# Kernel tuning notes

Hardware: AMD Instinct MI355X
Metric: run time of the kernel (lower is better)

Reference implementation:

```python
import math
import jax, jax.numpy as jnp
import numpy as np

B, T, C = 4, 2048, 1024
N_HEAD = 16
HEAD_DIM = C // N_HEAD

def setup_inputs() -> dict:
    key = jax.random.key(0)
    k0, k1, k2, k3, k4 = jax.random.split(key, 5)
    s = 1.0 / math.sqrt(C)
    return {
        "x": jax.random.normal(k0, (B, T, C), dtype=jnp.float32),
        "W_q": jax.random.normal(k1, (C, C), dtype=jnp.float32) * s,
        "W_k": jax.random.normal(k2, (C, C), dtype=jnp.float32) * s,
        "W_v": jax.random.normal(k3, (C, C), dtype=jnp.float32) * s,
        "W_o": jax.random.normal(k4, (C, C), dtype=jnp.float32) * s,
    }

def reference(x, W_q, W_k, W_v, W_o):
    b, t, c = x.shape
    h, hd = N_HEAD, HEAD_DIM
    # nn.Linear(y) = y @ W.T ; project and split heads -> [B, H, T, hd]
    q = (x @ W_q.T).reshape(b, t, h, hd).transpose(0, 2, 1, 3)
    k = (x @ W_k.T).reshape(b, t, h, hd).transpose(0, 2, 1, 3)
    v = (x @ W_v.T).reshape(b, t, h, hd).transpose(0, 2, 1, 3)
    # scores [B, H, T, T], causal mask, stable softmax
    attn = jnp.einsum('bhqd,bhkd->bhqk', q, k) / math.sqrt(hd)
    causal = jnp.tril(jnp.ones((t, t), dtype=bool))
    attn = jnp.where(causal[None, None], attn, -jnp.inf)
    attn = jax.nn.softmax(attn, axis=-1)
    out = jnp.einsum('bhqk,bhkd->bhqd', attn, v)
    out = out.transpose(0, 2, 1, 3).reshape(b, t, c)
    return out @ W_o.T
```

## Files before the change

kernel.cpp:

```cpp
#include <hip/hip_runtime.h>
#include <math.h>

#define Bsz 4
#define Tsz 2048
#define Csz 1024
#define NH  16
#define HD  64

typedef short bf16x8 __attribute__((ext_vector_type(8)));
typedef float f32x4  __attribute__((ext_vector_type(4)));
typedef unsigned short u16;
typedef unsigned int uint;

__device__ __forceinline__ u16 f2bf(float f) {
    union { float f; unsigned u; } v; v.f = f;
    unsigned r = v.u + 0x7fffu + ((v.u >> 16) & 1u);
    return (u16)(r >> 16);
}

__device__ __forceinline__ uint pkbf(float a, float b) {
    union { float f; uint u; } x, y; x.f = a; y.f = b;
    return ((x.u + 0x8000u) >> 16) | ((y.u + 0x8000u) & 0xFFFF0000u);
}

__device__ __forceinline__ void glds16(const u16* g, u16* l) {
    __builtin_amdgcn_global_load_lds(
        (const __attribute__((address_space(1))) void*)g,
        (__attribute__((address_space(3))) void*)l, 16, 0, 0);
}

__global__ void cast_all(const float* __restrict__ x,
                         const float* __restrict__ s0, const float* __restrict__ s1,
                         const float* __restrict__ s2, const float* __restrict__ s3,
                         u16* __restrict__ xb, u16* __restrict__ wdst) {
    const int NW = Csz * Csz;
    const size_t NX = (size_t)Bsz * Tsz * Csz;
    size_t i = ((size_t)blockIdx.x * blockDim.x + threadIdx.x) * 8;
    const float* src;
    u16* dst;
    if (i < NX) {
        src = x + i; dst = xb + i;
    } else {
        size_t j = i - NX;
        int m = (int)(j >> 20);
        size_t local = j & (NW - 1);
        src = ((m == 0) ? s0 : (m == 1) ? s1 : (m == 2) ? s2 : s3) + local;
        dst = wdst + j;
    }
    float4 a = *(const float4*)(src);
    float4 b = *(const float4*)(src + 4);
    bf16x8 o;
    o[0] = (short)f2bf(a.x); o[1] = (short)f2bf(a.y);
    o[2] = (short)f2bf(a.z); o[3] = (short)f2bf(a.w);
    o[4] = (short)f2bf(b.x); o[5] = (short)f2bf(b.y);
    o[6] = (short)f2bf(b.z); o[7] = (short)f2bf(b.w);
    *(bf16x8*)(dst) = o;
}


#define G2_SS 24576

#define G2_STAGEA(SLOT, KH, KT, PTR) {                                               \
    const int row_ = tid >> 2;                                                       \
    const int sc_ = (tid & 3) ^ ((row_ >> 1) & 3);                                   \
    glds16((PTR) + (size_t)row_ * 1024 + (KT) * 64 + (KH) * 32 + sc_ * 8,            \
           lds + (SLOT) * G2_SS + (KH) * 4096 + wave * 512); }

#define G2_STAGEB(SLOT, KH, KT, PTR) {                                               \
    _Pragma("unroll")                                                                \
    for (int rho = 0; rho < 2; rho++) {                                              \
        const int row_ = rho * 128 + (tid >> 2);                                     \
        const int sc_ = (tid & 3) ^ ((row_ >> 1) & 3);                               \
        glds16((PTR) + (size_t)row_ * 1024 + (KT) * 64 + (KH) * 32 + sc_ * 8,        \
               lds + (SLOT) * G2_SS + 8192 + (KH) * 8192 + rho * 4096 + wave * 512); } }

#define G2_PHASE(SLOT, KH, STAGE)                                                    \
    {                                                                                \
        __builtin_amdgcn_s_barrier();                                                \
        asm volatile("" ::: "memory");                                               \
        STAGE                                                                        \
        const u16* abase = lds + (SLOT) * G2_SS + (KH) * 4096;                       \
        const u16* bbase = lds + (SLOT) * G2_SS + 8192 + (KH) * 8192;                \
        bf16x8 afr[4], bfr[4];                                                       \
        _Pragma("unroll")                                                            \
        for (int i = 0; i < 4; i++) {                                                \
            const int ar = wrb + i * 16 + lr;                                        \
            afr[i] = *(const bf16x8*)(abase + ar * 32 +                              \
                                      ((lq ^ ((ar >> 1) & 3)) * 8));                 \
        }                                                                            \
        _Pragma("unroll")                                                            \
        for (int j = 0; j < 4; j++) {                                                \
            const int nr = wcb + j * 16 + lr;                                        \
            bfr[j] = *(const bf16x8*)(bbase + nr * 32 +                              \
                                      ((lq ^ ((nr >> 1) & 3)) * 8));                 \
        }                                                                            \
        asm volatile("" ::: "memory");                                               \
        __builtin_amdgcn_s_setprio(1);                                               \
        _Pragma("unroll")                                                            \
        for (int i = 0; i < 4; i++)                                                  \
            _Pragma("unroll")                                                        \
            for (int j = 0; j < 4; j++)                                              \
                acc[i][j] = __builtin_amdgcn_mfma_f32_16x16x32_bf16(                 \
                    afr[i], bfr[j], acc[i][j], 0, 0, 0);                             \
        __builtin_amdgcn_s_setprio(0);                                               \
    }

#define G2_VM(N) asm volatile("s_waitcnt vmcnt(" #N ")" ::: "memory")

#define G2_BODY(AP_, BP_)                                                            \
    __shared__ u16 lds[49152];                                                       \
    const int tid = threadIdx.x;                                                     \
    const int wave = tid >> 6, lane = tid & 63;                                      \
    const int lr = lane & 15, lq = lane >> 4;                                        \
    const int wrb = (wave >> 2) * 64, wcb = (wave & 3) * 64;                         \
    f32x4 acc[4][4] = {};                                                            \
    G2_STAGEA(0, 0, 0, AP_) G2_STAGEB(0, 0, 0, BP_)                                  \
    G2_STAGEA(0, 1, 0, AP_) G2_STAGEB(0, 1, 0, BP_)                                  \
    G2_STAGEA(1, 0, 1, AP_) G2_STAGEB(1, 0, 1, BP_)                                  \
    for (int t = 0; t < 16; t++) {                                                   \
        const int s = t & 1;                                                         \
        if (t == 15) { G2_VM(3); } else { G2_VM(6); }                                \
        G2_PHASE(s, 0, if (t < 15) { G2_STAGEA(s ^ 1, 1, t + 1, AP_)                 \
                                     G2_STAGEB(s ^ 1, 1, t + 1, BP_) })              \
        if (t == 15) { G2_VM(0); } else { G2_VM(6); }                                \
        G2_PHASE(s, 1, if (t < 14) { G2_STAGEA(s, 0, t + 2, AP_)                     \
                                     G2_STAGEB(s, 0, t + 2, BP_) })                  \
    }

__global__ __launch_bounds__(512, 2)
void gemm_qkv(const u16* __restrict__ A, const u16* __restrict__ Bm,
              u16* __restrict__ Qo, u16* __restrict__ Ko, u16* __restrict__ Vo,
              float qscale) {
    const int wg = blockIdx.x;
    const int chunk = wg & 7, pos = wg >> 3;
    const int m0 = ((chunk >> 1) * 16 + pos / 6) * 128;
    const int n0 = ((chunk & 1) * 6 + pos % 6) * 256;
    const u16* Ap = A  + (size_t)m0 * 1024;
    const u16* Bp = Bm + (size_t)n0 * 1024;

    G2_BODY(Ap, Bp)

    const int sel = n0 >> 10;
    if (sel == 2) {
        #pragma unroll
        for (int mi = 0; mi < 4; mi++) {
            #pragma unroll
            for (int ni = 0; ni < 4; ni++) {
                int m = m0 + wrb + mi * 16 + lq * 4;
                int b = m >> 11, tt = m & (Tsz - 1);
                int n = (n0 & 1023) + wcb + ni * 16 + lr;
                int h = n >> 6, d = n & (HD - 1);
                uint2 pk;
                pk.x = pkbf(acc[mi][ni][0], acc[mi][ni][1]);
                pk.y = pkbf(acc[mi][ni][2], acc[mi][ni][3]);
                *(uint2*)(&Vo[(((size_t)b * NH + h) * HD + d) * Tsz + tt]) = pk;
            }
        }
    } else {
        const float scale = (sel == 0) ? qscale : 1.0f;
        u16* dst = (sel == 0) ? Qo : Ko;
        #pragma unroll
        for (int mi = 0; mi < 4; mi++)
            #pragma unroll
            for (int ni = 0; ni < 4; ni++)
                #pragma unroll
                for (int r = 0; r < 4; r++) {
                    int m = m0 + wrb + mi * 16 + lq * 4 + r;
                    int n = (n0 & 1023) + wcb + ni * 16 + lr;
                    int b = m >> 11, tt = m & (Tsz - 1);
                    int h = n >> 6,  d = n & (HD - 1);
                    dst[(((size_t)b * NH + h) * Tsz + tt) * HD + d] = f2bf(acc[mi][ni][r] * scale);
                }
    }
}

__global__ __launch_bounds__(512, 2)
void gemm_out(const u16* __restrict__ A, const u16* __restrict__ Bm,
              float* __restrict__ out) {
    const int wg = blockIdx.x;
    const int chunk = wg & 7, pos = wg >> 3;
    const int m0 = (chunk * 8 + (pos >> 2)) * 128;
    const int n0 = (pos & 3) * 256;
    const u16* Ap = A  + (size_t)m0 * 1024;
    const u16* Bp = Bm + (size_t)n0 * 1024;

    G2_BODY(Ap, Bp)

    #pragma unroll
    for (int mi = 0; mi < 4; mi++)
        #pragma unroll
        for (int ni = 0; ni < 4; ni++)
            #pragma unroll
            for (int r = 0; r < 4; r++) {
                int m = m0 + wrb + mi * 16 + lq * 4 + r;
                int n = n0 + wcb + ni * 16 + lr;
                out[(size_t)m * Csz + n] = acc[mi][ni][r];
            }
}

#define LDT  72
#define LDTP 68

__global__ __launch_bounds__(256, 4)
void attn_kernel(const u16* __restrict__ Q, const u16* __restrict__ Kb,
                 const u16* __restrict__ Vt, u16* __restrict__ O) {
    __shared__ u16 sK[64 * LDT];
    __shared__ u16 sV[64 * LDT];
    __shared__ u16 sP[4][16 * LDTP];
    const int tid  = threadIdx.x;
    const int wave = tid >> 6, lane = tid & 63;
    const int lr = lane & 15, lq = lane >> 4;
    const int bh = blockIdx.x;
    const int qa = blockIdx.y;
    const int qc = 31 - qa;
    const int ta = qa * 64, tc = qc * 64;

    const u16* Qp = Q  + (size_t)bh * Tsz * HD;
    const u16* Kp = Kb + (size_t)bh * Tsz * HD;
    const u16* Vp = Vt + (size_t)bh * HD * Tsz;

    bf16x8 qfA0 = *(const bf16x8*)(Qp + (size_t)(ta + wave * 16 + lr) * HD + lq * 8);
    bf16x8 qfA1 = *(const bf16x8*)(Qp + (size_t)(ta + wave * 16 + lr) * HD + 32 + lq * 8);
    bf16x8 qfC0 = *(const bf16x8*)(Qp + (size_t)(tc + wave * 16 + lr) * HD + lq * 8);
    bf16x8 qfC1 = *(const bf16x8*)(Qp + (size_t)(tc + wave * 16 + lr) * HD + 32 + lq * 8);

    f32x4 accOA[4] = {}, accOC[4] = {};
    f32x4 accLA = {}, accLC = {};

    bf16x8 ones;
    #pragma unroll
    for (int i = 0; i < 8; i++) ones[i] = (short)0x3F80;

    const int strow = tid >> 3;
    const int stcol = (tid & 7) * 8;
    const u16* gK0 = Kp + (size_t)strow * HD + stcol;
    const u16* gK1 = gK0 + 32 * HD;
    const u16* gV0 = Vp + (size_t)strow * Tsz + stcol;
    const u16* gV1 = gV0 + 32 * Tsz;
    u16* lK0 = sK + strow * LDT + stcol;  u16* lK1 = lK0 + 32 * LDT;
    u16* lV0 = sV + strow * LDT + stcol;  u16* lV1 = lV0 + 32 * LDT;

    bf16x8 pK0 = *(const bf16x8*)(gK0);
    bf16x8 pK1 = *(const bf16x8*)(gK1);
    bf16x8 pV0 = *(const bf16x8*)(gV0);
    bf16x8 pV1 = *(const bf16x8*)(gV1);

#define PROCESS(T0, QF0, QF1, ACCO, ACCL, DIAG)                                       \
    {                                                                                 \
        f32x4 accS[4];                                                                \
        _Pragma("unroll")                                                             \
        for (int j = 0; j < 4; j++) {                                                 \
            bf16x8 b0 = *(const bf16x8*)(sK + (j * 16 + lr) * LDT + lq * 8);          \
            bf16x8 b1 = *(const bf16x8*)(sK + (j * 16 + lr) * LDT + 32 + lq * 8);     \
            f32x4 z = {};                                                             \
            z = __builtin_amdgcn_mfma_f32_16x16x32_bf16(QF0, b0, z, 0, 0, 0);         \
            z = __builtin_amdgcn_mfma_f32_16x16x32_bf16(QF1, b1, z, 0, 0, 0);         \
            accS[j] = z;                                                              \
        }                                                                             \
        _Pragma("unroll")                                                             \
        for (int r = 0; r < 4; r++) {                                                 \
            const int rowg = (T0) + wave * 16 + lq * 4 + r;                           \
            _Pragma("unroll")                                                         \
            for (int j = 0; j < 4; j++) {                                             \
                float v = accS[j][r];                                                 \
                if (DIAG && (kb * 64 + j * 16 + lr > rowg)) v = -200.0f;              \
                union { float f; uint u; } e;                                         \
                e.f = __builtin_amdgcn_exp2f(v);                                      \
                sP[wave][(lq * 4 + r) * LDTP + j * 16 + lr] = (u16)(e.u >> 16);       \
            }                                                                         \
        }                                                                             \
        _Pragma("unroll")                                                             \
        for (int ks = 0; ks < 2; ks++) {                                              \
            bf16x8 pf = *(const bf16x8*)(&sP[wave][0] + lr * LDTP + ks * 32 + lq * 8);\
            ACCL = __builtin_amdgcn_mfma_f32_16x16x32_bf16(pf, ones, ACCL, 0, 0, 0);  \
            _Pragma("unroll")                                                         \
            for (int j = 0; j < 4; j++) {                                             \
                bf16x8 vf = *(const bf16x8*)(sV + (j * 16 + lr) * LDT + ks * 32 + lq * 8); \
                ACCO[j] = __builtin_amdgcn_mfma_f32_16x16x32_bf16(pf, vf, ACCO[j], 0, 0, 0); \
            }                                                                         \
        }                                                                             \
    }

    for (int kb = 0; kb <= qc; kb++) {
        __syncthreads();
        *(bf16x8*)lK0 = pK0; *(bf16x8*)lK1 = pK1;
        *(bf16x8*)lV0 = pV0; *(bf16x8*)lV1 = pV1;
        __syncthreads();
        if (kb < qc) {
            pK0 = *(const bf16x8*)(gK0 + (size_t)(kb + 1) * 64 * HD);
            pK1 = *(const bf16x8*)(gK1 + (size_t)(kb + 1) * 64 * HD);
            pV0 = *(const bf16x8*)(gV0 + (kb + 1) * 64);
            pV1 = *(const bf16x8*)(gV1 + (kb + 1) * 64);
        }
        if (kb <= qa) PROCESS(ta, qfA0, qfA1, accOA, accLA, (kb == qa));
        PROCESS(tc, qfC0, qfC1, accOC, accLC, (kb == qc));
    }
#undef PROCESS

    const int b = bh >> 4, h = bh & 15;
    #pragma unroll
    for (int j = 0; j < 4; j++) {
        #pragma unroll
        for (int r = 0; r < 4; r++) {
            int t = wave * 16 + lq * 4 + r;
            int d = j * 16 + lr;
            O[((size_t)b * Tsz + ta + t) * Csz + h * HD + d] = f2bf(accOA[j][r] / accLA[r]);
            O[((size_t)b * Tsz + tc + t) * Csz + h * HD + d] = f2bf(accOC[j][r] / accLC[r]);
        }
    }
}

extern "C" void kernel_launch(void* const* d_in, const int* in_sizes, int n_in,
                              void* d_out, int out_size, void* d_ws, size_t ws_size,
                              hipStream_t stream) {
    const float* x  = (const float*)d_in[0];
    const float* Wq = (const float*)d_in[1];
    const float* Wk = (const float*)d_in[2];
    const float* Wv = (const float*)d_in[3];
    const float* Wo = (const float*)d_in[4];
    float* out = (float*)d_out;

    const size_t NX = (size_t)Bsz * Tsz * Csz;
    const size_t NW = (size_t)Csz * Csz;

    char* ws = (char*)d_ws;
    u16* xb   = (u16*)ws; ws += NX * 2;
    u16* wqkv = (u16*)ws; ws += 3 * NW * 2;
    u16* wob  = (u16*)ws; ws += NW * 2;
    u16* qbuf = (u16*)ws; ws += NX * 2;
    u16* kbuf = (u16*)ws; ws += NX * 2;
    u16* vtb  = (u16*)ws; ws += NX * 2;
    u16* abuf = (u16*)ws; ws += NX * 2;

    cast_all<<<dim3((unsigned)((NX + 4 * NW) / 2048)), 256, 0, stream>>>(
        x, Wq, Wk, Wv, Wo, xb, wqkv);

    const float qscale = 0.125f * 1.44269504088896340736f;
    gemm_qkv<<<dim3(768), 512, 0, stream>>>(xb, wqkv, qbuf, kbuf, vtb, qscale);

    attn_kernel<<<dim3(Bsz * NH, 16), 256, 0, stream>>>(qbuf, kbuf, vtb, abuf);

    gemm_out<<<dim3(256), 512, 0, stream>>>(abuf, wob, out);
}
```

Before: 241.9 us.

## Replace paired query-tile attention blocks with one tile per block

```diff
diff --git a/kernel.cpp b/kernel.cpp
--- a/kernel.cpp
+++ b/kernel.cpp
@@ -211,21 +211,18 @@
     const int wave = tid >> 6, lane = tid & 63;
     const int lr = lane & 15, lq = lane >> 4;
     const int bh = blockIdx.x;
-    const int qa = blockIdx.y;
-    const int qc = 31 - qa;
-    const int ta = qa * 64, tc = qc * 64;
+    const int tq = 31 - blockIdx.y;
+    const int tc = tq * 64;
 
     const u16* Qp = Q  + (size_t)bh * Tsz * HD;
     const u16* Kp = Kb + (size_t)bh * Tsz * HD;
     const u16* Vp = Vt + (size_t)bh * HD * Tsz;
 
-    bf16x8 qfA0 = *(const bf16x8*)(Qp + (size_t)(ta + wave * 16 + lr) * HD + lq * 8);
-    bf16x8 qfA1 = *(const bf16x8*)(Qp + (size_t)(ta + wave * 16 + lr) * HD + 32 + lq * 8);
-    bf16x8 qfC0 = *(const bf16x8*)(Qp + (size_t)(tc + wave * 16 + lr) * HD + lq * 8);
-    bf16x8 qfC1 = *(const bf16x8*)(Qp + (size_t)(tc + wave * 16 + lr) * HD + 32 + lq * 8);
-
-    f32x4 accOA[4] = {}, accOC[4] = {};
-    f32x4 accLA = {}, accLC = {};
+    bf16x8 qf0 = *(const bf16x8*)(Qp + (size_t)(tc + wave * 16 + lr) * HD + lq * 8);
+    bf16x8 qf1 = *(const bf16x8*)(Qp + (size_t)(tc + wave * 16 + lr) * HD + 32 + lq * 8);
+
+    f32x4 accO[4] = {};
+    f32x4 accL = {};
 
     bf16x8 ones;
     #pragma unroll
@@ -245,57 +242,53 @@
     bf16x8 pV0 = *(const bf16x8*)(gV0);
     bf16x8 pV1 = *(const bf16x8*)(gV1);
 
-#define PROCESS(T0, QF0, QF1, ACCO, ACCL, DIAG)                                       \
-    {                                                                                 \
-        f32x4 accS[4];                                                                \
-        _Pragma("unroll")                                                             \
-        for (int j = 0; j < 4; j++) {                                                 \
-            bf16x8 b0 = *(const bf16x8*)(sK + (j * 16 + lr) * LDT + lq * 8);          \
-            bf16x8 b1 = *(const bf16x8*)(sK + (j * 16 + lr) * LDT + 32 + lq * 8);     \
-            f32x4 z = {};                                                             \
-            z = __builtin_amdgcn_mfma_f32_16x16x32_bf16(QF0, b0, z, 0, 0, 0);         \
-            z = __builtin_amdgcn_mfma_f32_16x16x32_bf16(QF1, b1, z, 0, 0, 0);         \
-            accS[j] = z;                                                              \
-        }                                                                             \
-        _Pragma("unroll")                                                             \
-        for (int r = 0; r < 4; r++) {                                                 \
-            const int rowg = (T0) + wave * 16 + lq * 4 + r;                           \
-            _Pragma("unroll")                                                         \
-            for (int j = 0; j < 4; j++) {                                             \
-                float v = accS[j][r];                                                 \
-                if (DIAG && (kb * 64 + j * 16 + lr > rowg)) v = -200.0f;              \
-                union { float f; uint u; } e;                                         \
-                e.f = __builtin_amdgcn_exp2f(v);                                      \
-                sP[wave][(lq * 4 + r) * LDTP + j * 16 + lr] = (u16)(e.u >> 16);       \
-            }                                                                         \
-        }                                                                             \
-        _Pragma("unroll")                                                             \
-        for (int ks = 0; ks < 2; ks++) {                                              \
-            bf16x8 pf = *(const bf16x8*)(&sP[wave][0] + lr * LDTP + ks * 32 + lq * 8);\
-            ACCL = __builtin_amdgcn_mfma_f32_16x16x32_bf16(pf, ones, ACCL, 0, 0, 0);  \
-            _Pragma("unroll")                                                         \
-            for (int j = 0; j < 4; j++) {                                             \
-                bf16x8 vf = *(const bf16x8*)(sV + (j * 16 + lr) * LDT + ks * 32 + lq * 8); \
-                ACCO[j] = __builtin_amdgcn_mfma_f32_16x16x32_bf16(pf, vf, ACCO[j], 0, 0, 0); \
-            }                                                                         \
-        }                                                                             \
-    }
-
-    for (int kb = 0; kb <= qc; kb++) {
+    for (int kb = 0; kb <= tq; kb++) {
         __syncthreads();
         *(bf16x8*)lK0 = pK0; *(bf16x8*)lK1 = pK1;
         *(bf16x8*)lV0 = pV0; *(bf16x8*)lV1 = pV1;
         __syncthreads();
-        if (kb < qc) {
+        if (kb < tq) {
             pK0 = *(const bf16x8*)(gK0 + (size_t)(kb + 1) * 64 * HD);
             pK1 = *(const bf16x8*)(gK1 + (size_t)(kb + 1) * 64 * HD);
             pV0 = *(const bf16x8*)(gV0 + (kb + 1) * 64);
             pV1 = *(const bf16x8*)(gV1 + (kb + 1) * 64);
         }
-        if (kb <= qa) PROCESS(ta, qfA0, qfA1, accOA, accLA, (kb == qa));
-        PROCESS(tc, qfC0, qfC1, accOC, accLC, (kb == qc));
-    }
-#undef PROCESS
+        {
+            const int DIAG = (kb == tq);
+            f32x4 accS[4];
+            #pragma unroll
+            for (int j = 0; j < 4; j++) {
+                bf16x8 b0 = *(const bf16x8*)(sK + (j * 16 + lr) * LDT + lq * 8);
+                bf16x8 b1 = *(const bf16x8*)(sK + (j * 16 + lr) * LDT + 32 + lq * 8);
+                f32x4 z = {};
+                z = __builtin_amdgcn_mfma_f32_16x16x32_bf16(qf0, b0, z, 0, 0, 0);
+                z = __builtin_amdgcn_mfma_f32_16x16x32_bf16(qf1, b1, z, 0, 0, 0);
+                accS[j] = z;
+            }
+            #pragma unroll
+            for (int r = 0; r < 4; r++) {
+                const int rowg = tc + wave * 16 + lq * 4 + r;
+                #pragma unroll
+                for (int j = 0; j < 4; j++) {
+                    float v = accS[j][r];
+                    if (DIAG && (kb * 64 + j * 16 + lr > rowg)) v = -200.0f;
+                    union { float f; uint u; } e;
+                    e.f = __builtin_amdgcn_exp2f(v);
+                    sP[wave][(lq * 4 + r) * LDTP + j * 16 + lr] = (u16)(e.u >> 16);
+                }
+            }
+            #pragma unroll
+            for (int ks = 0; ks < 2; ks++) {
+                bf16x8 pf = *(const bf16x8*)(&sP[wave][0] + lr * LDTP + ks * 32 + lq * 8);
+                accL = __builtin_amdgcn_mfma_f32_16x16x32_bf16(pf, ones, accL, 0, 0, 0);
+                #pragma unroll
+                for (int j = 0; j < 4; j++) {
+                    bf16x8 vf = *(const bf16x8*)(sV + (j * 16 + lr) * LDT + ks * 32 + lq * 8);
+                    accO[j] = __builtin_amdgcn_mfma_f32_16x16x32_bf16(pf, vf, accO[j], 0, 0, 0);
+                }
+            }
+        }
+    }
 
     const int b = bh >> 4, h = bh & 15;
     #pragma unroll
@@ -304,8 +297,7 @@
         for (int r = 0; r < 4; r++) {
             int t = wave * 16 + lq * 4 + r;
             int d = j * 16 + lr;
-            O[((size_t)b * Tsz + ta + t) * Csz + h * HD + d] = f2bf(accOA[j][r] / accLA[r]);
-            O[((size_t)b * Tsz + tc + t) * Csz + h * HD + d] = f2bf(accOC[j][r] / accLC[r]);
+            O[((size_t)b * Tsz + tc + t) * Csz + h * HD + d] = f2bf(accO[j][r] / accL[r]);
         }
     }
 }
@@ -338,7 +330,7 @@
     const float qscale = 0.125f * 1.44269504088896340736f;
     gemm_qkv<<<dim3(768), 512, 0, stream>>>(xb, wqkv, qbuf, kbuf, vtb, qscale);
 
-    attn_kernel<<<dim3(Bsz * NH, 16), 256, 0, stream>>>(qbuf, kbuf, vtb, abuf);
+    attn_kernel<<<dim3(Bsz * NH, 32), 256, 0, stream>>>(qbuf, kbuf, vtb, abuf);
 
     gemm_out<<<dim3(256), 512, 0, stream>>>(abuf, wob, out);
 }
```

Measured after the change: 240.6 us, median of 2. Within noise of the previous version (-0.5%).

## Split paired causal attention blocks into one query tile per block, heavy tiles first

Applied to the files above, without the earlier changes.

```diff
diff --git a/kernel.cpp b/kernel.cpp
--- a/kernel.cpp
+++ b/kernel.cpp
@@ -211,21 +211,18 @@
     const int wave = tid >> 6, lane = tid & 63;
     const int lr = lane & 15, lq = lane >> 4;
     const int bh = blockIdx.x;
-    const int qa = blockIdx.y;
-    const int qc = 31 - qa;
-    const int ta = qa * 64, tc = qc * 64;
+    const int tq = 31 - blockIdx.y;
+    const int tc = tq * 64;
 
     const u16* Qp = Q  + (size_t)bh * Tsz * HD;
     const u16* Kp = Kb + (size_t)bh * Tsz * HD;
     const u16* Vp = Vt + (size_t)bh * HD * Tsz;
 
-    bf16x8 qfA0 = *(const bf16x8*)(Qp + (size_t)(ta + wave * 16 + lr) * HD + lq * 8);
-    bf16x8 qfA1 = *(const bf16x8*)(Qp + (size_t)(ta + wave * 16 + lr) * HD + 32 + lq * 8);
-    bf16x8 qfC0 = *(const bf16x8*)(Qp + (size_t)(tc + wave * 16 + lr) * HD + lq * 8);
-    bf16x8 qfC1 = *(const bf16x8*)(Qp + (size_t)(tc + wave * 16 + lr) * HD + 32 + lq * 8);
-
-    f32x4 accOA[4] = {}, accOC[4] = {};
-    f32x4 accLA = {}, accLC = {};
+    bf16x8 qf0 = *(const bf16x8*)(Qp + (size_t)(tc + wave * 16 + lr) * HD + lq * 8);
+    bf16x8 qf1 = *(const bf16x8*)(Qp + (size_t)(tc + wave * 16 + lr) * HD + 32 + lq * 8);
+
+    f32x4 accO[4] = {};
+    f32x4 accL = {};
 
     bf16x8 ones;
     #pragma unroll
@@ -245,7 +242,9 @@
     bf16x8 pV0 = *(const bf16x8*)(gV0);
     bf16x8 pV1 = *(const bf16x8*)(gV1);
 
-#define PROCESS(T0, QF0, QF1, ACCO, ACCL, DIAG)                                       \
+    u16* sPw = &sP[wave][0];
+
+#define PROCESS_BODY(MASKED)                                                          \
     {                                                                                 \
         f32x4 accS[4];                                                                \
         _Pragma("unroll")                                                             \
@@ -253,49 +252,61 @@
             bf16x8 b0 = *(const bf16x8*)(sK + (j * 16 + lr) * LDT + lq * 8);          \
             bf16x8 b1 = *(const bf16x8*)(sK + (j * 16 + lr) * LDT + 32 + lq * 8);     \
             f32x4 z = {};                                                             \
-            z = __builtin_amdgcn_mfma_f32_16x16x32_bf16(QF0, b0, z, 0, 0, 0);         \
-            z = __builtin_amdgcn_mfma_f32_16x16x32_bf16(QF1, b1, z, 0, 0, 0);         \
+            z = __builtin_amdgcn_mfma_f32_16x16x32_bf16(b0, qf0, z, 0, 0, 0);         \
+            z = __builtin_amdgcn_mfma_f32_16x16x32_bf16(b1, qf1, z, 0, 0, 0);         \
             accS[j] = z;                                                              \
         }                                                                             \
         _Pragma("unroll")                                                             \
-        for (int r = 0; r < 4; r++) {                                                 \
-            const int rowg = (T0) + wave * 16 + lq * 4 + r;                           \
-            _Pragma("unroll")                                                         \
-            for (int j = 0; j < 4; j++) {                                             \
-                float v = accS[j][r];                                                 \
-                if (DIAG && (kb * 64 + j * 16 + lr > rowg)) v = -200.0f;              \
-                union { float f; uint u; } e;                                         \
-                e.f = __builtin_amdgcn_exp2f(v);                                      \
-                sP[wave][(lq * 4 + r) * LDTP + j * 16 + lr] = (u16)(e.u >> 16);       \
+        for (int j = 0; j < 4; j++) {                                                 \
+            uint2 pk;                                                                 \
+            union { float f; uint u; } e0, e1, e2, e3;                                \
+            float v0 = accS[j][0], v1 = accS[j][1];                                   \
+            float v2 = accS[j][2], v3 = accS[j][3];                                   \
+            if (MASKED) {                                                             \
+                const int qrow = wave * 16 + lr;                                      \
+                const int kcol = j * 16 + lq * 4;                                     \
+                if (kcol + 0 > qrow) v0 = -200.0f;                                    \
+                if (kcol + 1 > qrow) v1 = -200.0f;                                    \
+                if (kcol + 2 > qrow) v2 = -200.0f;                                    \
+                if (kcol + 3 > qrow) v3 = -200.0f;                                    \
             }                                                                         \
+            e0.f = __builtin_amdgcn_exp2f(v0);                                        \
+            e1.f = __builtin_amdgcn_exp2f(v1);                                        \
+            e2.f = __builtin_amdgcn_exp2f(v2);                                        \
+            e3.f = __builtin_amdgcn_exp2f(v3);                                        \
+            pk.x = (e0.u >> 16) | (e1.u & 0xFFFF0000u);                               \
+            pk.y = (e2.u >> 16) | (e3.u & 0xFFFF0000u);                               \
+            *(uint2*)(sPw + lr * LDTP + j * 16 + lq * 4) = pk;                        \
         }                                                                             \
         _Pragma("unroll")                                                             \
         for (int ks = 0; ks < 2; ks++) {                                              \
-            bf16x8 pf = *(const bf16x8*)(&sP[wave][0] + lr * LDTP + ks * 32 + lq * 8);\
-            ACCL = __builtin_amdgcn_mfma_f32_16x16x32_bf16(pf, ones, ACCL, 0, 0, 0);  \
+            bf16x8 pf = *(const bf16x8*)(sPw + lr * LDTP + ks * 32 + lq * 8);         \
+            accL = __builtin_amdgcn_mfma_f32_16x16x32_bf16(pf, ones, accL, 0, 0, 0);  \
             _Pragma("unroll")                                                         \
             for (int j = 0; j < 4; j++) {                                             \
                 bf16x8 vf = *(const bf16x8*)(sV + (j * 16 + lr) * LDT + ks * 32 + lq * 8); \
-                ACCO[j] = __builtin_amdgcn_mfma_f32_16x16x32_bf16(pf, vf, ACCO[j], 0, 0, 0); \
+                accO[j] = __builtin_amdgcn_mfma_f32_16x16x32_bf16(pf, vf, accO[j], 0, 0, 0); \
             }                                                                         \
         }                                                                             \
     }
 
-    for (int kb = 0; kb <= qc; kb++) {
+    for (int kb = 0; kb < tq; kb++) {
         __syncthreads();
         *(bf16x8*)lK0 = pK0; *(bf16x8*)lK1 = pK1;
         *(bf16x8*)lV0 = pV0; *(bf16x8*)lV1 = pV1;
         __syncthreads();
-        if (kb < qc) {
-            pK0 = *(const bf16x8*)(gK0 + (size_t)(kb + 1) * 64 * HD);
-            pK1 = *(const bf16x8*)(gK1 + (size_t)(kb + 1) * 64 * HD);
-            pV0 = *(const bf16x8*)(gV0 + (kb + 1) * 64);
-            pV1 = *(const bf16x8*)(gV1 + (kb + 1) * 64);
-        }
-        if (kb <= qa) PROCESS(ta, qfA0, qfA1, accOA, accLA, (kb == qa));
-        PROCESS(tc, qfC0, qfC1, accOC, accLC, (kb == qc));
-    }
-#undef PROCESS
+        pK0 = *(const bf16x8*)(gK0 + (size_t)(kb + 1) * 64 * HD);
+        pK1 = *(const bf16x8*)(gK1 + (size_t)(kb + 1) * 64 * HD);
+        pV0 = *(const bf16x8*)(gV0 + (kb + 1) * 64);
+        pV1 = *(const bf16x8*)(gV1 + (kb + 1) * 64);
+        PROCESS_BODY(0)
+    }
+    __syncthreads();
+    *(bf16x8*)lK0 = pK0; *(bf16x8*)lK1 = pK1;
+    *(bf16x8*)lV0 = pV0; *(bf16x8*)lV1 = pV1;
+    __syncthreads();
+    PROCESS_BODY(1)
+#undef PROCESS_BODY
 
     const int b = bh >> 4, h = bh & 15;
     #pragma unroll
@@ -304,8 +315,7 @@
         for (int r = 0; r < 4; r++) {
             int t = wave * 16 + lq * 4 + r;
             int d = j * 16 + lr;
-            O[((size_t)b * Tsz + ta + t) * Csz + h * HD + d] = f2bf(accOA[j][r] / accLA[r]);
-            O[((size_t)b * Tsz + tc + t) * Csz + h * HD + d] = f2bf(accOC[j][r] / accLC[r]);
+            O[((size_t)b * Tsz + tc + t) * Csz + h * HD + d] = f2bf(accO[j][r] / accL[r]);
         }
     }
 }
@@ -338,7 +348,7 @@
     const float qscale = 0.125f * 1.44269504088896340736f;
     gemm_qkv<<<dim3(768), 512, 0, stream>>>(xb, wqkv, qbuf, kbuf, vtb, qscale);
 
-    attn_kernel<<<dim3(Bsz * NH, 16), 256, 0, stream>>>(qbuf, kbuf, vtb, abuf);
+    attn_kernel<<<dim3(Bsz * NH, 32), 256, 0, stream>>>(qbuf, kbuf, vtb, abuf);
 
     gemm_out<<<dim3(256), 512, 0, stream>>>(abuf, wob, out);
 }
```

New measurement: 267.9 us. +10.7%, slower.
